# Kernel tuning notes

Hardware: AMD Instinct MI355X
Metric: run time of the kernel (lower is better)

The kernel has to match this reference:

```python
import jax, jax.numpy as jnp
from jax import lax
import numpy as np

N, T, D, H, HG, OG = 2048, 256, 16, 256, 256, 128

def setup_inputs() -> dict:
    key = jax.random.key(0)
    ks = jax.random.split(key, 16)
    s = 0.05
    return {
        'x':    jax.random.normal(ks[0], (N, T, D), jnp.float32),
        'Wih0': jax.random.normal(ks[1], (4 * H, D), jnp.float32) * s,
        'Whh0': jax.random.normal(ks[2], (4 * H, H), jnp.float32) * s,
        'bih0': jax.random.normal(ks[3], (4 * H,), jnp.float32) * s,
        'bhh0': jax.random.normal(ks[4], (4 * H,), jnp.float32) * s,
        'Wih1': jax.random.normal(ks[5], (4 * H, H), jnp.float32) * s,
        'Whh1': jax.random.normal(ks[6], (4 * H, H), jnp.float32) * s,
        'bih1': jax.random.normal(ks[7], (4 * H,), jnp.float32) * s,
        'bhh1': jax.random.normal(ks[8], (4 * H,), jnp.float32) * s,
        'Wg1':  jax.random.normal(ks[9], (H, HG), jnp.float32) * s,
        'Wg2':  jax.random.normal(ks[10], (HG, OG), jnp.float32) * s,
        'Wfc':  jax.random.normal(ks[11], (OG, 1), jnp.float32) * s,
        'bfc':  jax.random.normal(ks[12], (1,), jnp.float32) * s,
    }

def lstm_layer(x, Wih, Whh, bih, bhh):
    # x: [N, T, Din]; torch gate order i, f, g, o stacked along 4H
    n = x.shape[0]
    h4 = Whh.shape[0]
    hid = h4 // 4
    xg = jnp.einsum('ntd,gd->ntg', x, Wih) + bih + bhh  # precompute input part
    def step(carry, g_t):
        h, c = carry
        g = g_t + h @ Whh.T
        i, f, gg, o = jnp.split(g, 4, axis=-1)
        c = jax.nn.sigmoid(f) * c + jax.nn.sigmoid(i) * jnp.tanh(gg)
        h = jax.nn.sigmoid(o) * jnp.tanh(c)
        return (h, c), h
    h0 = jnp.zeros((n, hid), x.dtype)
    (_, _), hs = lax.scan(step, (h0, h0), jnp.swapaxes(xg, 0, 1))
    return jnp.swapaxes(hs, 0, 1)  # [N, T, H]

def adjacency(nf):
    # detached correlation graph + symmetric degree normalization
    f = lax.stop_gradient(nf)
    xc = f - f.mean(axis=1, keepdims=True)
    cov = xc @ xc.T
    d = jnp.sqrt(jnp.diag(cov))
    corr = jnp.nan_to_num(jnp.clip(cov / (d[:, None] * d[None, :]), -1.0, 1.0))
    A = corr + jnp.eye(f.shape[0], dtype=f.dtype)
    dinv = jnp.power(A.sum(axis=1), -0.5)
    dinv = jnp.where(jnp.isinf(dinv), 0.0, dinv)
    return dinv[:, None] * A * dinv[None, :]

def reference(x, Wih0, Whh0, bih0, bhh0, Wih1, Whh1, bih1, bhh1, Wg1, Wg2, Wfc, bfc):
    h = lstm_layer(x, Wih0, Whh0, bih0, bhh0)
    h = lstm_layer(h, Wih1, Whh1, bih1, bhh1)
    nf = h[:, -1, :]                      # [N, H]
    adj = adjacency(nf)                   # [N, N]
    g1 = jax.nn.relu(adj @ (nf @ Wg1))    # GCN layer 1 (dropout=0, eval)
    g2 = adj @ (g1 @ Wg2)                 # GCN layer 2
    pred = g2 @ Wfc + bfc                 # [N, 1]
    return pred[:, 0]
```

## Files before the change

### kernel.cpp

```cpp
#include <hip/hip_runtime.h>
#include <hip/hip_bf16.h>
#include <cmath>

#define NN 2048
#define TT 256
#define DD 16
#define HH 256

typedef __attribute__((ext_vector_type(8))) short short8;
typedef __attribute__((ext_vector_type(4))) float f32x4;

__device__ __forceinline__ float sigmoidf_(float x){ return 1.0f/(1.0f+expf(-x)); }

__device__ __forceinline__ void glds16(const __hip_bfloat16* g, __hip_bfloat16* l){
  __builtin_amdgcn_global_load_lds(
      (const __attribute__((address_space(1))) void*)g,
      (__attribute__((address_space(3))) void*)l, 16, 0, 0);
}

__global__ __launch_bounds__(256) void pack_w2(const float* __restrict__ W,
                                               __hip_bfloat16* __restrict__ P){
  int tid = blockIdx.x*256 + threadIdx.x;
  int r = tid >> 8, k = tid & 255;
  float w = W[tid];
  __hip_bfloat16 h = __float2bfloat16(w);
  __hip_bfloat16 l = __float2bfloat16(w - __bfloat162float(h));
  size_t base = (size_t)r*512;
  P[base + k] = h; P[base + 256 + k] = l;
}
__global__ __launch_bounds__(256) void pack_w0(const float* __restrict__ W,
                                               __hip_bfloat16* __restrict__ P){
  int tid = blockIdx.x*256 + threadIdx.x;
  int r = tid >> 4, k = tid & 15;
  float w = W[tid];
  __hip_bfloat16 h = __float2bfloat16(w);
  __hip_bfloat16 l = __float2bfloat16(w - __bfloat162float(h));
  size_t base = (size_t)r*64;
  P[base + k] = h; P[base + 16 + k] = h; P[base + 32 + k] = l;
  P[base + 48 + k] = __float2bfloat16(0.0f);
}
__global__ __launch_bounds__(256) void pack_x(const float* __restrict__ x,
                                              __hip_bfloat16* __restrict__ Xp){
  int tid = blockIdx.x*256 + threadIdx.x;
  const float* xr = x + (size_t)tid*16;
  __hip_bfloat16* o = Xp + (size_t)tid*64;
  for (int k=0;k<16;k++){
    float v = xr[k];
    __hip_bfloat16 h = __float2bfloat16(v);
    __hip_bfloat16 l = __float2bfloat16(v - __bfloat162float(h));
    o[k] = h; o[16+k] = l; o[32+k] = h; o[48+k] = __float2bfloat16(0.0f);
  }
}
__global__ __launch_bounds__(256) void recon_nf(const __hip_bfloat16* __restrict__ hi,
    const __hip_bfloat16* __restrict__ lo, float* __restrict__ nf){
  int tid = blockIdx.x*256 + threadIdx.x;
  nf[tid] = __bfloat162float(hi[tid]) + __bfloat162float(lo[tid]);
}

__device__ __forceinline__ void mm_merged(
    const __hip_bfloat16* __restrict__ Ahi, const __hip_bfloat16* __restrict__ Alo,
    size_t lda,
    const __hip_bfloat16* __restrict__ Bhi, const __hip_bfloat16* __restrict__ Blo,
    size_t ldb, int Klen,
    int m0, int j0, int wv, int lane, int rr, int sw8, int frow,
    f32x4 (&acc)[2][4],
    __hip_bfloat16* AsH, __hip_bfloat16* AsL,
    __hip_bfloat16* BsH, __hip_bfloat16* BsL)
{
  const size_t arow = (size_t)(m0 + wv*32 + rr)*lda + sw8;
  const size_t brow = (size_t)(wv*256 + j0 + rr)*ldb + sw8;
  for (int kb=0; kb<Klen; kb+=64){
    {
      const __hip_bfloat16* AbH = Ahi + arow + kb;
      __hip_bfloat16* AdH = AsH + (wv*32)*64;
      #pragma unroll
      for (int c2=0;c2<4;c2++) glds16(AbH + (size_t)(c2*8)*lda, AdH + c2*8*64);
      const __hip_bfloat16* AbL = Alo + arow + kb;
      __hip_bfloat16* AdL = AsL + (wv*32)*64;
      #pragma unroll
      for (int c2=0;c2<4;c2++) glds16(AbL + (size_t)(c2*8)*lda, AdL + c2*8*64);
      const __hip_bfloat16* Bb1 = Bhi + brow + kb;
      __hip_bfloat16* Bd1 = BsH + (wv<<4)*64;
      glds16(Bb1, Bd1); glds16(Bb1 + (size_t)8*ldb, Bd1 + 8*64);
      const __hip_bfloat16* Bb2 = Blo + brow + kb;
      __hip_bfloat16* Bd2 = BsL + (wv<<4)*64;
      glds16(Bb2, Bd2); glds16(Bb2 + (size_t)8*ldb, Bd2 + 8*64);
    }
    __syncthreads();
    #pragma unroll
    for (int w2=0; w2<2; ++w2){
      const int sl8 = ((((w2<<2) + (lane>>4)) ^ (lane&7)) << 3);
      short8 ah0 = *(const short8*)&AsH[(wv*32 +      frow)*64 + sl8];
      short8 ah1 = *(const short8*)&AsH[(wv*32 + 16 + frow)*64 + sl8];
      short8 al0 = *(const short8*)&AsL[(wv*32 +      frow)*64 + sl8];
      short8 al1 = *(const short8*)&AsL[(wv*32 + 16 + frow)*64 + sl8];
      #pragma unroll
      for (int g=0; g<4; ++g){
        short8 bh = *(const short8*)&BsH[((g<<4) + frow)*64 + sl8];
        acc[0][g] = __builtin_amdgcn_mfma_f32_16x16x32_bf16(ah0, bh, acc[0][g], 0,0,0);
        acc[1][g] = __builtin_amdgcn_mfma_f32_16x16x32_bf16(ah1, bh, acc[1][g], 0,0,0);
        acc[0][g] = __builtin_amdgcn_mfma_f32_16x16x32_bf16(al0, bh, acc[0][g], 0,0,0);
        acc[1][g] = __builtin_amdgcn_mfma_f32_16x16x32_bf16(al1, bh, acc[1][g], 0,0,0);
        short8 bl = *(const short8*)&BsL[((g<<4) + frow)*64 + sl8];
        acc[0][g] = __builtin_amdgcn_mfma_f32_16x16x32_bf16(ah0, bl, acc[0][g], 0,0,0);
        acc[1][g] = __builtin_amdgcn_mfma_f32_16x16x32_bf16(ah1, bl, acc[1][g], 0,0,0);
      }
    }
    __syncthreads();
  }
}

__device__ __forceinline__ void mm_single64(
    const __hip_bfloat16* __restrict__ A, size_t lda,
    const __hip_bfloat16* __restrict__ B, size_t ldb,
    int m0, int j0, int wv, int lane, int rr, int sw8, int frow,
    f32x4 (&acc)[2][4],
    __hip_bfloat16* As0, __hip_bfloat16* Bh0)
{
  {
    const __hip_bfloat16* Ab = A + (size_t)(m0 + wv*32 + rr)*lda + sw8;
    __hip_bfloat16* Ad = As0 + (wv*32)*64;
    #pragma unroll
    for (int c2=0;c2<4;c2++) glds16(Ab + (size_t)(c2*8)*lda, Ad + c2*8*64);
    const __hip_bfloat16* Bb1 = B + (size_t)(wv*256 + j0 + rr)*ldb + sw8;
    __hip_bfloat16* Bd1 = Bh0 + (wv<<4)*64;
    glds16(Bb1, Bd1); glds16(Bb1 + (size_t)8*ldb, Bd1 + 8*64);
  }
  __syncthreads();
  #pragma unroll
  for (int w2=0; w2<2; ++w2){
    const int sl8 = ((((w2<<2) + (lane>>4)) ^ (lane&7)) << 3);
    short8 a0 = *(const short8*)&As0[(wv*32 +      frow)*64 + sl8];
    short8 a1 = *(const short8*)&As0[(wv*32 + 16 + frow)*64 + sl8];
    #pragma unroll
    for (int g=0; g<4; ++g){
      short8 b1 = *(const short8*)&Bh0[((g<<4) + frow)*64 + sl8];
      acc[0][g] = __builtin_amdgcn_mfma_f32_16x16x32_bf16(a0, b1, acc[0][g], 0,0,0);
      acc[1][g] = __builtin_amdgcn_mfma_f32_16x16x32_bf16(a1, b1, acc[1][g], 0,0,0);
    }
  }
  __syncthreads();
}

__global__ __launch_bounds__(256, 2) void lstm2_step(
    int t,
    const __hip_bfloat16* __restrict__ Xp,
    const __hip_bfloat16* __restrict__ P0ih,
    const __hip_bfloat16* __restrict__ P0hh,
    const __hip_bfloat16* __restrict__ P1ih,
    const __hip_bfloat16* __restrict__ P1hh,
    const float* __restrict__ bih0, const float* __restrict__ bhh0,
    const float* __restrict__ bih1, const float* __restrict__ bhh1,
    const __hip_bfloat16* __restrict__ h0p_hi, const __hip_bfloat16* __restrict__ h0p_lo,
    __hip_bfloat16* __restrict__ h0o_hi, __hip_bfloat16* __restrict__ h0o_lo,
    const __hip_bfloat16* __restrict__ h1p_hi, const __hip_bfloat16* __restrict__ h1p_lo,
    __hip_bfloat16* __restrict__ h1o_hi, __hip_bfloat16* __restrict__ h1o_lo,
    float* __restrict__ c0, float* __restrict__ c1)
{
  __shared__ __align__(16) __hip_bfloat16 AsH[128*64];
  __shared__ __align__(16) __hip_bfloat16 AsL[128*64];
  __shared__ __align__(16) __hip_bfloat16 BsH[64*64];
  __shared__ __align__(16) __hip_bfloat16 BsL[64*64];

  const int bid = blockIdx.x;
  const int xcd = bid & 7;
  const int slot = bid >> 3;
  const bool isL0 = xcd < 4;
  if (isL0 && t >= TT) return;
  if (!isL0 && t == 0) return;
  const int lg = isL0 ? xcd : (xcd - 4);
  const int jg = ((lg & 1) << 3) + (slot & 7);
  const int mg = ((lg >> 1) << 3) + (slot >> 3);
  const int m0 = mg << 7;
  const int j0 = jg << 4;
  const int lane = threadIdx.x & 63, wv = threadIdx.x >> 6;
  const int rr = lane >> 3;
  const int sw8 = (((lane & 7) ^ rr) << 3);
  const int frow = lane & 15;

  f32x4 acc[2][4] = {};

  if (isL0){
    if (t != 0){
      mm_merged(h0p_hi, h0p_lo, 256, P0hh, P0hh+256, 512, 256,
                m0, j0, wv, lane, rr, sw8, frow, acc, AsH, AsL, BsH, BsL);
    }
    mm_single64(Xp + (size_t)t*64, (size_t)TT*64, P0ih, 64,
                m0, j0, wv, lane, rr, sw8, frow, acc, AsH, BsH);
  } else {
    mm_merged(h0p_hi, h0p_lo, 256, P1ih, P1ih+256, 512, 256,
              m0, j0, wv, lane, rr, sw8, frow, acc, AsH, AsL, BsH, BsL);
    if (t != 1){
      mm_merged(h1p_hi, h1p_lo, 256, P1hh, P1hh+256, 512, 256,
                m0, j0, wv, lane, rr, sw8, frow, acc, AsH, AsL, BsH, BsL);
    }
  }

  const int j = j0 + frow;
  const float* bih = isL0 ? bih0 : bih1;
  const float* bhh = isL0 ? bhh0 : bhh1;
  float* cst = isL0 ? c0 : c1;
  __hip_bfloat16* ohi = isL0 ? h0o_hi : h1o_hi;
  __hip_bfloat16* olo = isL0 ? h0o_lo : h1o_lo;
  const int first = isL0 ? (t==0) : (t==1);
  const float b0 = bih[j]        + bhh[j];
  const float b1 = bih[HH + j]   + bhh[HH + j];
  const float b2 = bih[2*HH + j] + bhh[2*HH + j];
  const float b3 = bih[3*HH + j] + bhh[3*HH + j];
  #pragma unroll
  for (int mt=0; mt<2; ++mt){
    const int mrb = m0 + wv*32 + mt*16 + ((lane>>4)<<2);
    #pragma unroll
    for (int r=0; r<4; ++r){
      const size_t mi = (size_t)(mrb + r)*HH + j;
      float gi = acc[mt][0][r] + b0;
      float gf = acc[mt][1][r] + b1;
      float gg = acc[mt][2][r] + b2;
      float go = acc[mt][3][r] + b3;
      float cold = first ? 0.f : cst[mi];
      float cn = sigmoidf_(gf)*cold + sigmoidf_(gi)*tanhf(gg);
      float hv = sigmoidf_(go)*tanhf(cn);
      cst[mi] = cn;
      __hip_bfloat16 hb = __float2bfloat16(hv);
      ohi[mi] = hb;
      olo[mi] = __float2bfloat16(hv - __bfloat162float(hb));
    }
  }
}

__global__ __launch_bounds__(256) void gemm_nn(
    float* __restrict__ C, const float* __restrict__ A, const float* __restrict__ B,
    int K, int lda, int ldb, int ldc, int relu)
{
  __shared__ float As_[16][68];
  __shared__ float Bs_[16][64];
  float acc[4][4] = {};
  const int tx = threadIdx.x;
  const int m0 = blockIdx.y<<6, n0 = blockIdx.x<<6;
  const int am = tx>>2, ak = (tx&3)<<2;
  const int bk = tx>>4, bn = (tx&15)<<2;
  const int mm = (tx>>4)<<2, nc = (tx&15)<<2;
  for (int kb=0; kb<K; kb+=16){
    float4 av = *reinterpret_cast<const float4*>(A + (size_t)(m0+am)*lda + kb + ak);
    As_[ak][am]=av.x; As_[ak+1][am]=av.y; As_[ak+2][am]=av.z; As_[ak+3][am]=av.w;
    *reinterpret_cast<float4*>(&Bs_[bk][bn]) =
      *reinterpret_cast<const float4*>(B + (size_t)(kb+bk)*ldb + n0 + bn);
    __syncthreads();
    #pragma unroll
    for (int k=0;k<16;k++){
      float4 a4 = *reinterpret_cast<const float4*>(&As_[k][mm]);
      float4 b4 = *reinterpret_cast<const float4*>(&Bs_[k][nc]);
      acc[0][0]=fmaf(a4.x,b4.x,acc[0][0]); acc[0][1]=fmaf(a4.x,b4.y,acc[0][1]);
      acc[0][2]=fmaf(a4.x,b4.z,acc[0][2]); acc[0][3]=fmaf(a4.x,b4.w,acc[0][3]);
      acc[1][0]=fmaf(a4.y,b4.x,acc[1][0]); acc[1][1]=fmaf(a4.y,b4.y,acc[1][1]);
      acc[1][2]=fmaf(a4.y,b4.z,acc[1][2]); acc[1][3]=fmaf(a4.y,b4.w,acc[1][3]);
      acc[2][0]=fmaf(a4.z,b4.x,acc[2][0]); acc[2][1]=fmaf(a4.z,b4.y,acc[2][1]);
      acc[2][2]=fmaf(a4.z,b4.z,acc[2][2]); acc[2][3]=fmaf(a4.z,b4.w,acc[2][3]);
      acc[3][0]=fmaf(a4.w,b4.x,acc[3][0]); acc[3][1]=fmaf(a4.w,b4.y,acc[3][1]);
      acc[3][2]=fmaf(a4.w,b4.z,acc[3][2]); acc[3][3]=fmaf(a4.w,b4.w,acc[3][3]);
    }
    __syncthreads();
  }
  #pragma unroll
  for (int r=0;r<4;r++){
    float4 v = make_float4(acc[r][0],acc[r][1],acc[r][2],acc[r][3]);
    if (relu){ v.x=fmaxf(v.x,0.f); v.y=fmaxf(v.y,0.f); v.z=fmaxf(v.z,0.f); v.w=fmaxf(v.w,0.f); }
    *reinterpret_cast<float4*>(C + (size_t)(m0+mm+r)*ldc + n0 + nc) = v;
  }
}

__global__ __launch_bounds__(256) void gemm_nt(
    float* __restrict__ C, const float* __restrict__ A, const float* __restrict__ B,
    int K, int lda, int ldb, int ldc)
{
  __shared__ float As_[16][68];
  __shared__ float Bs_[16][68];
  float acc[4][4] = {};
  const int tx = threadIdx.x;
  const int m0 = blockIdx.y<<6, n0 = blockIdx.x<<6;
  const int am = tx>>2, ak = (tx&3)<<2;
  const int mm = (tx>>4)<<2, nc = (tx&15)<<2;
  for (int kb=0; kb<K; kb+=16){
    float4 av = *reinterpret_cast<const float4*>(A + (size_t)(m0+am)*lda + kb + ak);
    As_[ak][am]=av.x; As_[ak+1][am]=av.y; As_[ak+2][am]=av.z; As_[ak+3][am]=av.w;
    float4 bv = *reinterpret_cast<const float4*>(B + (size_t)(n0+am)*ldb + kb + ak);
    Bs_[ak][am]=bv.x; Bs_[ak+1][am]=bv.y; Bs_[ak+2][am]=bv.z; Bs_[ak+3][am]=bv.w;
    __syncthreads();
    #pragma unroll
    for (int k=0;k<16;k++){
      float4 a4 = *reinterpret_cast<const float4*>(&As_[k][mm]);
      float4 b4 = *reinterpret_cast<const float4*>(&Bs_[k][nc]);
      acc[0][0]=fmaf(a4.x,b4.x,acc[0][0]); acc[0][1]=fmaf(a4.x,b4.y,acc[0][1]);
      acc[0][2]=fmaf(a4.x,b4.z,acc[0][2]); acc[0][3]=fmaf(a4.x,b4.w,acc[0][3]);
      acc[1][0]=fmaf(a4.y,b4.x,acc[1][0]); acc[1][1]=fmaf(a4.y,b4.y,acc[1][1]);
      acc[1][2]=fmaf(a4.y,b4.z,acc[1][2]); acc[1][3]=fmaf(a4.y,b4.w,acc[1][3]);
      acc[2][0]=fmaf(a4.z,b4.x,acc[2][0]); acc[2][1]=fmaf(a4.z,b4.y,acc[2][1]);
      acc[2][2]=fmaf(a4.z,b4.z,acc[2][2]); acc[2][3]=fmaf(a4.z,b4.w,acc[2][3]);
      acc[3][0]=fmaf(a4.w,b4.x,acc[3][0]); acc[3][1]=fmaf(a4.w,b4.y,acc[3][1]);
      acc[3][2]=fmaf(a4.w,b4.z,acc[3][2]); acc[3][3]=fmaf(a4.w,b4.w,acc[3][3]);
    }
    __syncthreads();
  }
  #pragma unroll
  for (int r=0;r<4;r++){
    float4 v = make_float4(acc[r][0],acc[r][1],acc[r][2],acc[r][3]);
    *reinterpret_cast<float4*>(C + (size_t)(m0+mm+r)*ldc + n0 + nc) = v;
  }
}

__global__ __launch_bounds__(256) void rowstat(const float* __restrict__ nf,
    float* __restrict__ xc, float* __restrict__ dvec)
{
  __shared__ float red[256];
  int n = blockIdx.x, tx = threadIdx.x;
  float v = nf[(size_t)n*HH + tx];
  red[tx] = v; __syncthreads();
  for (int s=128; s>0; s>>=1){ if (tx<s) red[tx]+=red[tx+s]; __syncthreads(); }
  float mean = red[0] * (1.0f/HH);
  __syncthreads();
  float d = v - mean;
  xc[(size_t)n*HH + tx] = d;
  red[tx] = d*d; __syncthreads();
  for (int s=128; s>0; s>>=1){ if (tx<s) red[tx]+=red[tx+s]; __syncthreads(); }
  if (tx==0) dvec[n] = sqrtf(red[0]);
}

__global__ __launch_bounds__(256) void rowsum(const float* __restrict__ cov,
    const float* __restrict__ dvec, float* __restrict__ dinv)
{
  __shared__ float red[256];
  int i = blockIdx.x, tx = threadIdx.x;
  float di = dvec[i];
  float s = 0.f;
  for (int jj=tx; jj<NN; jj+=256){
    float r = cov[(size_t)i*NN + jj] / (di * dvec[jj]);
    if (r != r) r = 0.f; else r = fminf(1.f, fmaxf(-1.f, r));
    s += r;
  }
  red[tx]=s; __syncthreads();
  for (int st=128; st>0; st>>=1){ if (tx<st) red[tx]+=red[tx+st]; __syncthreads(); }
  if (tx==0){
    float tot = red[0] + 1.0f;
    float p = powf(tot, -0.5f);
    if (isinf(p)) p = 0.f;
    dinv[i] = p;
  }
}

__global__ __launch_bounds__(256) void adjnorm(float* __restrict__ cov,
    const float* __restrict__ dvec, const float* __restrict__ dinv)
{
  size_t idx = (size_t)blockIdx.x*256 + threadIdx.x;
  int i = (int)(idx >> 11), jj = (int)(idx & (NN-1));
  float r = cov[idx] / (dvec[i]*dvec[jj]);
  if (r != r) r = 0.f; else r = fminf(1.f, fmaxf(-1.f, r));
  if (i==jj) r += 1.f;
  cov[idx] = dinv[i]*r*dinv[jj];
}

__global__ __launch_bounds__(128) void predk(const float* __restrict__ G2,
    const float* __restrict__ Wfc, const float* __restrict__ bfc, float* __restrict__ out)
{
  int n = blockIdx.x, tx = threadIdx.x;
  float v = G2[(size_t)n*128 + tx] * Wfc[tx];
  for (int off=32; off>0; off>>=1) v += __shfl_down(v, off);
  __shared__ float p[2];
  if ((tx&63)==0) p[tx>>6] = v;
  __syncthreads();
  if (tx==0) out[n] = p[0] + p[1] + bfc[0];
}

extern "C" void kernel_launch(void* const* d_in, const int* in_sizes, int n_in,
                              void* d_out, int out_size, void* d_ws, size_t ws_size,
                              hipStream_t stream)
{
  const float* x    = (const float*)d_in[0];
  const float* Wih0 = (const float*)d_in[1];
  const float* Whh0 = (const float*)d_in[2];
  const float* bih0 = (const float*)d_in[3];
  const float* bhh0 = (const float*)d_in[4];
  const float* Wih1 = (const float*)d_in[5];
  const float* Whh1 = (const float*)d_in[6];
  const float* bih1 = (const float*)d_in[7];
  const float* bhh1 = (const float*)d_in[8];
  const float* Wg1  = (const float*)d_in[9];
  const float* Wg2  = (const float*)d_in[10];
  const float* Wfc  = (const float*)d_in[11];
  const float* bfc  = (const float*)d_in[12];
  float* out = (float*)d_out;

  char* w = (char*)d_ws;
  auto alloc = [&](size_t bytes){ char* p = w; w += (bytes + 255) & ~(size_t)255; return p; };
  __hip_bfloat16* Xp   = (__hip_bfloat16*)alloc((size_t)NN*TT*64*2);
  __hip_bfloat16* P0hh = (__hip_bfloat16*)alloc((size_t)1024*512*2);
  __hip_bfloat16* P1ih = (__hip_bfloat16*)alloc((size_t)1024*512*2);
  __hip_bfloat16* P1hh = (__hip_bfloat16*)alloc((size_t)1024*512*2);
  __hip_bfloat16* P0ih = (__hip_bfloat16*)alloc((size_t)1024*64*2);
  __hip_bfloat16 *H0hi[2], *H0lo[2], *H1hi[2], *H1lo[2];
  for (int i=0;i<2;i++){ H0hi[i]=(__hip_bfloat16*)alloc((size_t)NN*HH*2);
                         H0lo[i]=(__hip_bfloat16*)alloc((size_t)NN*HH*2); }
  for (int i=0;i<2;i++){ H1hi[i]=(__hip_bfloat16*)alloc((size_t)NN*HH*2);
                         H1lo[i]=(__hip_bfloat16*)alloc((size_t)NN*HH*2); }
  float* c0   = (float*)alloc((size_t)NN*HH*4);
  float* c1   = (float*)alloc((size_t)NN*HH*4);
  float* nf   = (float*)alloc((size_t)NN*HH*4);
  float* xc   = (float*)alloc((size_t)NN*HH*4);
  float* cov  = (float*)alloc((size_t)NN*NN*4);
  float* t1   = (float*)alloc((size_t)NN*HH*4);
  float* G1   = (float*)alloc((size_t)NN*HH*4);
  float* t2   = (float*)alloc((size_t)NN*128*4);
  float* G2   = (float*)alloc((size_t)NN*128*4);
  float* dvec = (float*)alloc((size_t)NN*4);
  float* dinv = (float*)alloc((size_t)NN*4);

  hipLaunchKernelGGL(pack_w2, dim3(1024), dim3(256), 0, stream, Whh0, P0hh);
  hipLaunchKernelGGL(pack_w2, dim3(1024), dim3(256), 0, stream, Wih1, P1ih);
  hipLaunchKernelGGL(pack_w2, dim3(1024), dim3(256), 0, stream, Whh1, P1hh);
  hipLaunchKernelGGL(pack_w0, dim3(64),   dim3(256), 0, stream, Wih0, P0ih);
  hipLaunchKernelGGL(pack_x,  dim3(2048), dim3(256), 0, stream, x, Xp);

  for (int t=0; t<=TT; ++t){
    const __hip_bfloat16 *h0p_hi = H0hi[(t+1)&1], *h0p_lo = H0lo[(t+1)&1];
    __hip_bfloat16 *h0o_hi = H0hi[t&1], *h0o_lo = H0lo[t&1];
    const __hip_bfloat16 *h1p_hi = H1hi[t&1], *h1p_lo = H1lo[t&1];
    __hip_bfloat16 *h1o_hi = H1hi[(t+1)&1], *h1o_lo = H1lo[(t+1)&1];
    hipLaunchKernelGGL(lstm2_step, dim3(512), dim3(256), 0, stream,
        t, Xp, P0ih, P0hh, P1ih, P1hh, bih0, bhh0, bih1, bhh1,
        h0p_hi, h0p_lo, h0o_hi, h0o_lo, h1p_hi, h1p_lo, h1o_hi, h1o_lo, c0, c1);
  }
  hipLaunchKernelGGL(recon_nf, dim3(2048), dim3(256), 0, stream, H1hi[1], H1lo[1], nf);

  hipLaunchKernelGGL(rowstat, dim3(NN), dim3(256), 0, stream, nf, xc, dvec);
  hipLaunchKernelGGL(gemm_nt, dim3(NN/64, NN/64), dim3(256), 0, stream,
      cov, xc, xc, HH, HH, HH, NN);
  hipLaunchKernelGGL(rowsum, dim3(NN), dim3(256), 0, stream, cov, dvec, dinv);
  hipLaunchKernelGGL(adjnorm, dim3(NN*NN/256), dim3(256), 0, stream, cov, dvec, dinv);

  hipLaunchKernelGGL(gemm_nn, dim3(HH/64, NN/64), dim3(256), 0, stream,
      t1, nf, Wg1, HH, HH, HH, HH, 0);
  hipLaunchKernelGGL(gemm_nn, dim3(HH/64, NN/64), dim3(256), 0, stream,
      G1, cov, t1, NN, NN, HH, HH, 1);
  hipLaunchKernelGGL(gemm_nn, dim3(128/64, NN/64), dim3(256), 0, stream,
      t2, G1, Wg2, HH, HH, 128, 128, 0);
  hipLaunchKernelGGL(gemm_nn, dim3(128/64, NN/64), dim3(256), 0, stream,
      G2, cov, t2, NN, NN, 128, 128, 0);
  hipLaunchKernelGGL(predk, dim3(NN), dim3(128), 0, stream, G2, Wfc, bfc, out);
}
```

Before: 4.844 ms.

## Load A fragments straight to registers and double-buffer B tiles in LDS

The A-operand (hidden-state hi/lo) fragments are now read from global memory directly into registers in MFMA fragment layout, instead of being staged through LDS. Loads for the next K chunk are prefetched into a second register set, and B weight tiles go into two alternating LDS buffers. This removes the trailing barrier of each K iteration and lets the next chunk's loads overlap the current MFMAs. It also shrinks shared memory from 48KB to 32KB per block. In exchange it uses more VGPRs for the prefetched fragments and issues uncoalesced 16-byte global loads for A, which may limit occupancy or add memory latency.

```diff
diff --git a/kernel.cpp b/kernel.cpp
--- a/kernel.cpp
+++ b/kernel.cpp
@@ -11,6 +11,10 @@
 typedef __attribute__((ext_vector_type(4))) float f32x4;
 
 __device__ __forceinline__ float sigmoidf_(float x){ return 1.0f/(1.0f+expf(-x)); }
+
+__device__ __forceinline__ short8 ld8bf(const __hip_bfloat16* p){
+  return *reinterpret_cast<const short8*>(p);
+}
 
 __device__ __forceinline__ void glds16(const __hip_bfloat16* g, __hip_bfloat16* l){
   __builtin_amdgcn_global_load_lds(
@@ -61,52 +65,73 @@
     const __hip_bfloat16* __restrict__ Ahi, const __hip_bfloat16* __restrict__ Alo,
     size_t lda,
     const __hip_bfloat16* __restrict__ Bhi, const __hip_bfloat16* __restrict__ Blo,
-    size_t ldb, int Klen,
+    size_t ldb,
     int m0, int j0, int wv, int lane, int rr, int sw8, int frow,
     f32x4 (&acc)[2][4],
-    __hip_bfloat16* AsH, __hip_bfloat16* AsL,
-    __hip_bfloat16* BsH, __hip_bfloat16* BsL)
-{
-  const size_t arow = (size_t)(m0 + wv*32 + rr)*lda + sw8;
+    __hip_bfloat16* BsH0, __hip_bfloat16* BsL0,
+    __hip_bfloat16* BsH1, __hip_bfloat16* BsL1)
+{
   const size_t brow = (size_t)(wv*256 + j0 + rr)*ldb + sw8;
-  for (int kb=0; kb<Klen; kb+=64){
-    {
-      const __hip_bfloat16* AbH = Ahi + arow + kb;
-      __hip_bfloat16* AdH = AsH + (wv*32)*64;
+  const int aoff = ((lane>>4)<<3);
+  const size_t ar0 = (size_t)(m0 + wv*32 + frow)*lda + aoff;
+  const size_t ar1 = ar0 + (size_t)16*lda;
+
+  short8 pah0[2][2], pah1[2][2], pal0[2][2], pal1[2][2];
+
+  #pragma unroll
+  for (int w2=0; w2<2; ++w2){
+    pah0[0][w2] = ld8bf(Ahi + ar0 + w2*32);
+    pah1[0][w2] = ld8bf(Ahi + ar1 + w2*32);
+    pal0[0][w2] = ld8bf(Alo + ar0 + w2*32);
+    pal1[0][w2] = ld8bf(Alo + ar1 + w2*32);
+  }
+  {
+    const __hip_bfloat16* Bb1 = Bhi + brow;
+    __hip_bfloat16* Bd1 = BsH0 + (wv<<4)*64;
+    glds16(Bb1, Bd1); glds16(Bb1 + (size_t)8*ldb, Bd1 + 8*64);
+    const __hip_bfloat16* Bb2 = Blo + brow;
+    __hip_bfloat16* Bd2 = BsL0 + (wv<<4)*64;
+    glds16(Bb2, Bd2); glds16(Bb2 + (size_t)8*ldb, Bd2 + 8*64);
+  }
+
+  #pragma unroll
+  for (int c=0; c<4; ++c){
+    __syncthreads();
+    if (c < 3){
+      const int kb = (c+1)*64;
+      const int pn = (c+1)&1;
       #pragma unroll
-      for (int c2=0;c2<4;c2++) glds16(AbH + (size_t)(c2*8)*lda, AdH + c2*8*64);
-      const __hip_bfloat16* AbL = Alo + arow + kb;
-      __hip_bfloat16* AdL = AsL + (wv*32)*64;
-      #pragma unroll
-      for (int c2=0;c2<4;c2++) glds16(AbL + (size_t)(c2*8)*lda, AdL + c2*8*64);
+      for (int w2=0; w2<2; ++w2){
+        pah0[pn][w2] = ld8bf(Ahi + ar0 + kb + w2*32);
+        pah1[pn][w2] = ld8bf(Ahi + ar1 + kb + w2*32);
+        pal0[pn][w2] = ld8bf(Alo + ar0 + kb + w2*32);
+        pal1[pn][w2] = ld8bf(Alo + ar1 + kb + w2*32);
+      }
+      __hip_bfloat16* BdH = (pn ? BsH1 : BsH0) + (wv<<4)*64;
+      __hip_bfloat16* BdL = (pn ? BsL1 : BsL0) + (wv<<4)*64;
       const __hip_bfloat16* Bb1 = Bhi + brow + kb;
-      __hip_bfloat16* Bd1 = BsH + (wv<<4)*64;
-      glds16(Bb1, Bd1); glds16(Bb1 + (size_t)8*ldb, Bd1 + 8*64);
+      glds16(Bb1, BdH); glds16(Bb1 + (size_t)8*ldb, BdH + 8*64);
       const __hip_bfloat16* Bb2 = Blo + brow + kb;
-      __hip_bfloat16* Bd2 = BsL + (wv<<4)*64;
-      glds16(Bb2, Bd2); glds16(Bb2 + (size_t)8*ldb, Bd2 + 8*64);
-    }
-    __syncthreads();
+      glds16(Bb2, BdL); glds16(Bb2 + (size_t)8*ldb, BdL + 8*64);
+    }
+    const int p = c&1;
+    const __hip_bfloat16* BH = p ? BsH1 : BsH0;
+    const __hip_bfloat16* BL = p ? BsL1 : BsL0;
     #pragma unroll
     for (int w2=0; w2<2; ++w2){
       const int sl8 = ((((w2<<2) + (lane>>4)) ^ (lane&7)) << 3);
-      short8 ah0 = *(const short8*)&AsH[(wv*32 +      frow)*64 + sl8];
-      short8 ah1 = *(const short8*)&AsH[(wv*32 + 16 + frow)*64 + sl8];
-      short8 al0 = *(const short8*)&AsL[(wv*32 +      frow)*64 + sl8];
-      short8 al1 = *(const short8*)&AsL[(wv*32 + 16 + frow)*64 + sl8];
       #pragma unroll
       for (int g=0; g<4; ++g){
-        short8 bh = *(const short8*)&BsH[((g<<4) + frow)*64 + sl8];
-        acc[0][g] = __builtin_amdgcn_mfma_f32_16x16x32_bf16(ah0, bh, acc[0][g], 0,0,0);
-        acc[1][g] = __builtin_amdgcn_mfma_f32_16x16x32_bf16(ah1, bh, acc[1][g], 0,0,0);
-        acc[0][g] = __builtin_amdgcn_mfma_f32_16x16x32_bf16(al0, bh, acc[0][g], 0,0,0);
-        acc[1][g] = __builtin_amdgcn_mfma_f32_16x16x32_bf16(al1, bh, acc[1][g], 0,0,0);
-        short8 bl = *(const short8*)&BsL[((g<<4) + frow)*64 + sl8];
-        acc[0][g] = __builtin_amdgcn_mfma_f32_16x16x32_bf16(ah0, bl, acc[0][g], 0,0,0);
-        acc[1][g] = __builtin_amdgcn_mfma_f32_16x16x32_bf16(ah1, bl, acc[1][g], 0,0,0);
+        short8 bh = ld8bf(&BH[((g<<4) + frow)*64 + sl8]);
+        acc[0][g] = __builtin_amdgcn_mfma_f32_16x16x32_bf16(pah0[p][w2], bh, acc[0][g], 0,0,0);
+        acc[1][g] = __builtin_amdgcn_mfma_f32_16x16x32_bf16(pah1[p][w2], bh, acc[1][g], 0,0,0);
+        acc[0][g] = __builtin_amdgcn_mfma_f32_16x16x32_bf16(pal0[p][w2], bh, acc[0][g], 0,0,0);
+        acc[1][g] = __builtin_amdgcn_mfma_f32_16x16x32_bf16(pal1[p][w2], bh, acc[1][g], 0,0,0);
+        short8 bl = ld8bf(&BL[((g<<4) + frow)*64 + sl8]);
+        acc[0][g] = __builtin_amdgcn_mfma_f32_16x16x32_bf16(pah0[p][w2], bl, acc[0][g], 0,0,0);
+        acc[1][g] = __builtin_amdgcn_mfma_f32_16x16x32_bf16(pah1[p][w2], bl, acc[1][g], 0,0,0);
       }
     }
-    __syncthreads();
   }
 }
 
@@ -115,13 +140,18 @@
     const __hip_bfloat16* __restrict__ B, size_t ldb,
     int m0, int j0, int wv, int lane, int rr, int sw8, int frow,
     f32x4 (&acc)[2][4],
-    __hip_bfloat16* As0, __hip_bfloat16* Bh0)
-{
+    __hip_bfloat16* Bh0)
+{
+  const int aoff = ((lane>>4)<<3);
+  const size_t ar0 = (size_t)(m0 + wv*32 + frow)*lda + aoff;
+  const size_t ar1 = ar0 + (size_t)16*lda;
+  short8 a0[2], a1[2];
+  #pragma unroll
+  for (int w2=0; w2<2; ++w2){
+    a0[w2] = ld8bf(A + ar0 + w2*32);
+    a1[w2] = ld8bf(A + ar1 + w2*32);
+  }
   {
-    const __hip_bfloat16* Ab = A + (size_t)(m0 + wv*32 + rr)*lda + sw8;
-    __hip_bfloat16* Ad = As0 + (wv*32)*64;
-    #pragma unroll
-    for (int c2=0;c2<4;c2++) glds16(Ab + (size_t)(c2*8)*lda, Ad + c2*8*64);
     const __hip_bfloat16* Bb1 = B + (size_t)(wv*256 + j0 + rr)*ldb + sw8;
     __hip_bfloat16* Bd1 = Bh0 + (wv<<4)*64;
     glds16(Bb1, Bd1); glds16(Bb1 + (size_t)8*ldb, Bd1 + 8*64);
@@ -130,16 +160,13 @@
   #pragma unroll
   for (int w2=0; w2<2; ++w2){
     const int sl8 = ((((w2<<2) + (lane>>4)) ^ (lane&7)) << 3);
-    short8 a0 = *(const short8*)&As0[(wv*32 +      frow)*64 + sl8];
-    short8 a1 = *(const short8*)&As0[(wv*32 + 16 + frow)*64 + sl8];
     #pragma unroll
     for (int g=0; g<4; ++g){
-      short8 b1 = *(const short8*)&Bh0[((g<<4) + frow)*64 + sl8];
-      acc[0][g] = __builtin_amdgcn_mfma_f32_16x16x32_bf16(a0, b1, acc[0][g], 0,0,0);
-      acc[1][g] = __builtin_amdgcn_mfma_f32_16x16x32_bf16(a1, b1, acc[1][g], 0,0,0);
-    }
-  }
-  __syncthreads();
+      short8 b1 = ld8bf(&Bh0[((g<<4) + frow)*64 + sl8]);
+      acc[0][g] = __builtin_amdgcn_mfma_f32_16x16x32_bf16(a0[w2], b1, acc[0][g], 0,0,0);
+      acc[1][g] = __builtin_amdgcn_mfma_f32_16x16x32_bf16(a1[w2], b1, acc[1][g], 0,0,0);
+    }
+  }
 }
 
 __global__ __launch_bounds__(256, 2) void lstm2_step(
@@ -157,10 +184,10 @@
     __hip_bfloat16* __restrict__ h1o_hi, __hip_bfloat16* __restrict__ h1o_lo,
     float* __restrict__ c0, float* __restrict__ c1)
 {
-  __shared__ __align__(16) __hip_bfloat16 AsH[128*64];
-  __shared__ __align__(16) __hip_bfloat16 AsL[128*64];
-  __shared__ __align__(16) __hip_bfloat16 BsH[64*64];
-  __shared__ __align__(16) __hip_bfloat16 BsL[64*64];
+  __shared__ __align__(16) __hip_bfloat16 BsH0[64*64];
+  __shared__ __align__(16) __hip_bfloat16 BsL0[64*64];
+  __shared__ __align__(16) __hip_bfloat16 BsH1[64*64];
+  __shared__ __align__(16) __hip_bfloat16 BsL1[64*64];
 
   const int bid = blockIdx.x;
   const int xcd = bid & 7;
@@ -182,17 +209,17 @@
 
   if (isL0){
     if (t != 0){
-      mm_merged(h0p_hi, h0p_lo, 256, P0hh, P0hh+256, 512, 256,
-                m0, j0, wv, lane, rr, sw8, frow, acc, AsH, AsL, BsH, BsL);
+      mm_merged(h0p_hi, h0p_lo, 256, P0hh, P0hh+256, 512,
+                m0, j0, wv, lane, rr, sw8, frow, acc, BsH0, BsL0, BsH1, BsL1);
     }
     mm_single64(Xp + (size_t)t*64, (size_t)TT*64, P0ih, 64,
-                m0, j0, wv, lane, rr, sw8, frow, acc, AsH, BsH);
+                m0, j0, wv, lane, rr, sw8, frow, acc, BsH0);
   } else {
-    mm_merged(h0p_hi, h0p_lo, 256, P1ih, P1ih+256, 512, 256,
-              m0, j0, wv, lane, rr, sw8, frow, acc, AsH, AsL, BsH, BsL);
+    mm_merged(h0p_hi, h0p_lo, 256, P1ih, P1ih+256, 512,
+              m0, j0, wv, lane, rr, sw8, frow, acc, BsH0, BsL0, BsH1, BsL1);
     if (t != 1){
-      mm_merged(h1p_hi, h1p_lo, 256, P1hh, P1hh+256, 512, 256,
-                m0, j0, wv, lane, rr, sw8, frow, acc, AsH, AsL, BsH, BsL);
+      mm_merged(h1p_hi, h1p_lo, 256, P1hh, P1hh+256, 512,
+                m0, j0, wv, lane, rr, sw8, frow, acc, BsH0, BsL0, BsH1, BsL1);
     }
   }
 
```

After: 6.401 ms. 32.1% more time.
